# Optimization experiments

Hardware: AMD Instinct MI355X
Metric: run time of the kernel (lower is better)

## Reference

```python
import math
import jax, jax.numpy as jnp
import numpy as np

B, H, S, D = 2, 16, 2048, 64

def setup_inputs() -> dict:
    key = jax.random.key(0)
    kq, kk, kv = jax.random.split(key, 3)
    return {
        "query": jax.random.normal(kq, (B, H, S, D), dtype=jnp.float32),
        "key": jax.random.normal(kk, (B, H, S, D), dtype=jnp.float32),
        "value": jax.random.normal(kv, (B, H, S, D), dtype=jnp.float32),
        "mask": jnp.ones((B, S, 1), dtype=jnp.float32),  # padding mask, 1 = keep
        "mask_now": 0,  # 0 -> causal (tril diag=0); 1 -> strict causal (diag=-1)
    }

def reference(query, key, value, mask, mask_now):
    d_k = query.shape[-1]
    seq_len = mask.shape[1]
    # [B,H,S,S] scaled scores
    attn_scores = jnp.einsum("bhqd,bhkd->bhqk", query, key) / math.sqrt(d_k)
    diag = -1 if mask_now else 0
    triu_mask = jnp.tril(jnp.ones((seq_len, seq_len), dtype=mask.dtype), diag)  # [S,S]
    # mask[:, :, 0] -> per-query padding mask broadcast over key dim: [B,1,S,S]
    full_mask = triu_mask[None, None, :, :] * mask[:, None, :, 0:1]
    attn_scores = jnp.where(full_mask == 0, jnp.float32(-1e9), attn_scores)
    attn_scores = jax.nn.softmax(attn_scores, axis=-1)
    output = jnp.einsum("bhqk,bhkd->bhqd", attn_scores, value)
    return (output, attn_scores)
```

## Files before the change

### kernel.cpp

```cpp
#include <hip/hip_runtime.h>
#include <math.h>

#define NB 2
#define NH 16
#define SL 2048
#define DD 64
#define KC 64
#define NCH (SL / KC)
#define NT 256
#define LPS 68

typedef short bf16x8 __attribute__((ext_vector_type(8)));
typedef float f32x4  __attribute__((ext_vector_type(4)));

__device__ __forceinline__ unsigned short f2bf(float x) {
    unsigned u = __float_as_uint(x);
    u += 0x7fffu + ((u >> 16) & 1u);
    return (unsigned short)(u >> 16);
}

__device__ __forceinline__ void lds_barrier() {
    asm volatile("s_waitcnt lgkmcnt(0)\n\ts_barrier" ::: "memory");
}

__global__ __launch_bounds__(256)
void cvt_bf16(const float* __restrict__ in, unsigned short* __restrict__ out,
              int n4, float scale)
{
    int i = blockIdx.x * 256 + threadIdx.x;
    if (i >= n4) return;
    float4 v = ((const float4*)in)[i];
    ushort4 o;
    o.x = f2bf(v.x * scale); o.y = f2bf(v.y * scale);
    o.z = f2bf(v.z * scale); o.w = f2bf(v.w * scale);
    ((ushort4*)out)[i] = o;
}

__global__ __launch_bounds__(256)
void transpose_v(const float* __restrict__ V, unsigned short* __restrict__ Vt)
{
    __shared__ __align__(16) unsigned short vt[64 * 72];
    const int bh = blockIdx.x >> 5;
    const int s0 = (blockIdx.x & 31) * 64;
    const int t  = threadIdx.x;

    const float4* src = (const float4*)(V + ((size_t)bh * SL + s0) * DD);
    #pragma unroll
    for (int i = 0; i < 4; ++i) {
        int idx = t + i * 256;
        int r = idx >> 4, d4 = idx & 15;
        float4 v = src[r * 16 + d4];
        vt[(d4 * 4 + 0) * 72 + r] = f2bf(v.x);
        vt[(d4 * 4 + 1) * 72 + r] = f2bf(v.y);
        vt[(d4 * 4 + 2) * 72 + r] = f2bf(v.z);
        vt[(d4 * 4 + 3) * 72 + r] = f2bf(v.w);
    }
    __syncthreads();
    const int d = t >> 2, seg = t & 3;
    unsigned short* dst = Vt + ((size_t)bh * DD + d) * SL + s0 + seg * 16;
    uint4 p0 = *(const uint4*)&vt[d * 72 + seg * 16];
    uint4 p1 = *(const uint4*)&vt[d * 72 + seg * 16 + 8];
    *(uint4*)dst = p0;
    *(uint4*)(dst + 8) = p1;
}

__global__ __launch_bounds__(NT, 8)
void attn_mfma(const unsigned short* __restrict__ Qb,
               const unsigned short* __restrict__ Kb,
               const unsigned short* __restrict__ Vt,
               const float* __restrict__ Mg,
               const int* __restrict__ MNg,
               float* __restrict__ Og)
{
    __shared__ __align__(16) float ps[4][16 * LPS];
    __shared__ float lsx[4][16];

    const int tid  = threadIdx.x;
    const int w    = tid >> 6;
    const int lane = tid & 63;
    const int l15  = lane & 15;
    const int qd   = lane >> 4;

    const int lin  = blockIdx.x;
    const int xcd  = lin & 7;
    const int iloc = lin >> 3;
    const int bh   = xcd * 4 + (iloc >> 6);
    const int g    = iloc & 63;
    const int j    = (iloc >> 5) & 7;
    const int b    = bh >> 4;

    const int role  = (w + j) & 3;
    const int khalf = role & 1;
    const int r0    = (role < 2) ? g * 16 : 2032 - g * 16;

    const int diag = (MNg[0] != 0) ? -1 : 0;

    int rlim[4]; int anyDeg = 0;
    #pragma unroll
    for (int reg = 0; reg < 4; ++reg) {
        int row = r0 + qd * 4 + reg;
        float m = Mg[(size_t)b * SL + row];
        int rl = row + diag;
        if (m == 0.0f) rl = -1;
        rlim[reg] = rl;
        anyDeg |= (rl < 0);
    }
    const bool grpDeg = __any(anyDeg);
    const int lastB = grpDeg ? (NCH - 1) : ((r0 + 15 + diag) >> 6);
    const int N     = lastB + 1;
    const int kcMid = N >> 1;
    const int kcBeg = khalf ? kcMid : 0;
    const int kcEnd = khalf ? N : kcMid;

    const unsigned short* Qh  = Qb + (size_t)bh * SL * DD;
    const unsigned short* Kh  = Kb + (size_t)bh * SL * DD;
    const unsigned short* Vth = Vt + (size_t)bh * DD * SL;
    float* Oo   = Og + ((size_t)bh * SL + r0) * DD;
    float* Sout = Og + (size_t)NB * NH * SL * DD
                     + (size_t)bh * SL * SL + (size_t)r0 * SL;
    float* slab = ps[role];

    const unsigned short* qrow = Qh + (size_t)(r0 + l15) * DD + qd * 8;
    bf16x8 qf0 = *(const bf16x8*)qrow;
    bf16x8 qf1 = *(const bf16x8*)(qrow + 32);

    float lacc[4] = {0.0f, 0.0f, 0.0f, 0.0f};
    for (int it = kcBeg * 4; it < kcEnd * 4; ++it) {
        const unsigned short* kr = Kh + (size_t)(it * 16 + l15) * DD + qd * 8;
        bf16x8 f0 = *(const bf16x8*)kr;
        bf16x8 f1 = *(const bf16x8*)(kr + 32);
        f32x4 acc = {0.0f, 0.0f, 0.0f, 0.0f};
        __builtin_amdgcn_s_setprio(1);
        acc = __builtin_amdgcn_mfma_f32_16x16x32_bf16(qf0, f0, acc, 0, 0, 0);
        acc = __builtin_amdgcn_mfma_f32_16x16x32_bf16(qf1, f1, acc, 0, 0, 0);
        __builtin_amdgcn_s_setprio(0);
        const int col = it * 16 + l15;
        #pragma unroll
        for (int reg = 0; reg < 4; ++reg)
            lacc[reg] += (col <= rlim[reg]) ? __builtin_exp2f(acc[reg]) : 0.0f;
    }

    float lsum[4];
    #pragma unroll
    for (int reg = 0; reg < 4; ++reg) {
        float s = lacc[reg];
        s += __shfl_xor(s, 1);  s += __shfl_xor(s, 2);
        s += __shfl_xor(s, 4);  s += __shfl_xor(s, 8);
        lsum[reg] = s;
    }
    if (l15 == 0) {
        #pragma unroll
        for (int reg = 0; reg < 4; ++reg)
            lsx[role][qd * 4 + reg] = lsum[reg];
    }
    lds_barrier();
    float pmul[4], pfill[4];
    #pragma unroll
    for (int reg = 0; reg < 4; ++reg) {
        float tot = lsum[reg] + lsx[role ^ 1][qd * 4 + reg];
        pmul[reg]  = (rlim[reg] < 0) ? 0.0f : 1.0f / tot;
        pfill[reg] = (rlim[reg] < 0) ? (1.0f / (float)SL) : 0.0f;
    }

    f32x4 oacc[4];
    #pragma unroll
    for (int nt = 0; nt < 4; ++nt) oacc[nt] = (f32x4){0.0f, 0.0f, 0.0f, 0.0f};

    for (int kc = kcBeg; kc < kcEnd; ++kc) {
        const int c0 = kc * KC;
        #pragma unroll
        for (int nt = 0; nt < 4; ++nt) {
            const unsigned short* kr = Kh + (size_t)(c0 + nt * 16 + l15) * DD + qd * 8;
            bf16x8 f0 = *(const bf16x8*)kr;
            bf16x8 f1 = *(const bf16x8*)(kr + 32);
            f32x4 acc = {0.0f, 0.0f, 0.0f, 0.0f};
            __builtin_amdgcn_s_setprio(1);
            acc = __builtin_amdgcn_mfma_f32_16x16x32_bf16(qf0, f0, acc, 0, 0, 0);
            acc = __builtin_amdgcn_mfma_f32_16x16x32_bf16(qf1, f1, acc, 0, 0, 0);
            __builtin_amdgcn_s_setprio(0);
            const int col = c0 + nt * 16 + l15;
            #pragma unroll
            for (int reg = 0; reg < 4; ++reg) {
                float val = (col <= rlim[reg]) ? __builtin_exp2f(acc[reg]) * pmul[reg]
                                               : pfill[reg];
                slab[(qd * 4 + reg) * LPS + nt * 16 + l15] = val;
            }
        }
        #pragma unroll
        for (int ii = 0; ii < 4; ++ii) {
            int idx = ii * 64 + lane;
            int rr = idx >> 4, c4 = idx & 15;
            *(float4*)(Sout + (size_t)rr * SL + c0 + c4 * 4) =
                *(const float4*)&slab[rr * LPS + c4 * 4];
        }
        bf16x8 paf[2];
        #pragma unroll
        for (int kb = 0; kb < 2; ++kb) {
            const float* pr = &slab[l15 * LPS + kb * 32 + qd * 8];
            float4 x = *(const float4*)pr;
            float4 y = *(const float4*)(pr + 4);
            bf16x8 f;
            f[0] = (short)f2bf(x.x); f[1] = (short)f2bf(x.y);
            f[2] = (short)f2bf(x.z); f[3] = (short)f2bf(x.w);
            f[4] = (short)f2bf(y.x); f[5] = (short)f2bf(y.y);
            f[6] = (short)f2bf(y.z); f[7] = (short)f2bf(y.w);
            paf[kb] = f;
        }
        #pragma unroll
        for (int nt = 0; nt < 4; ++nt) {
            const unsigned short* vr = Vth + (size_t)(nt * 16 + l15) * SL + c0 + qd * 8;
            bf16x8 v0 = *(const bf16x8*)vr;
            bf16x8 v1 = *(const bf16x8*)(vr + 32);
            __builtin_amdgcn_s_setprio(1);
            oacc[nt] = __builtin_amdgcn_mfma_f32_16x16x32_bf16(paf[0], v0, oacc[nt], 0, 0, 0);
            oacc[nt] = __builtin_amdgcn_mfma_f32_16x16x32_bf16(paf[1], v1, oacc[nt], 0, 0, 0);
            __builtin_amdgcn_s_setprio(0);
        }
    }

    {
        const int zc0 = N * KC;
        const int rbeg = khalf * 8;
        float4 z = make_float4(0.0f, 0.0f, 0.0f, 0.0f);
        for (int rr = rbeg; rr < rbeg + 8; ++rr) {
            float* rowp = Sout + (size_t)rr * SL;
            for (int c = zc0 + (lane << 2); c < SL; c += 256)
                *(float4*)(rowp + c) = z;
        }
    }

    #pragma unroll
    for (int nt = 0; nt < 4; ++nt)
        #pragma unroll
        for (int reg = 0; reg < 4; ++reg)
            slab[(qd * 4 + reg) * LPS + nt * 16 + l15] = oacc[nt][reg];
    lds_barrier();
    {
        const float* sA = ps[role & ~1];
        const float* sB = ps[role | 1];
        #pragma unroll
        for (int ii = 0; ii < 2; ++ii) {
            int idx = ii * 64 + lane;
            int rr = (idx >> 4) + khalf * 8;
            int c4 = idx & 15;
            float4 a = *(const float4*)&sA[rr * LPS + c4 * 4];
            float4 bv = *(const float4*)&sB[rr * LPS + c4 * 4];
            float4 o = make_float4(a.x + bv.x, a.y + bv.y, a.z + bv.z, a.w + bv.w);
            *(float4*)(Oo + (size_t)rr * DD + c4 * 4) = o;
        }
    }
}

extern "C" void kernel_launch(void* const* d_in, const int* in_sizes, int n_in,
                              void* d_out, int out_size, void* d_ws, size_t ws_size,
                              hipStream_t stream)
{
    const float* q  = (const float*)d_in[0];
    const float* k  = (const float*)d_in[1];
    const float* v  = (const float*)d_in[2];
    const float* mk = (const float*)d_in[3];
    const int*   mn = (const int*)d_in[4];
    float* out = (float*)d_out;

    const size_t nElem = (size_t)NB * NH * SL * DD;
    unsigned short* Qb = (unsigned short*)d_ws;
    unsigned short* Kp = Qb + nElem;
    unsigned short* Vp = Kp + nElem;

    const int n4 = (int)(nElem / 4);
    cvt_bf16<<<n4 / 256, 256, 0, stream>>>(q, Qb, n4, 0.125f * 1.44269504f);
    cvt_bf16<<<n4 / 256, 256, 0, stream>>>(k, Kp, n4, 1.0f);
    transpose_v<<<NB * NH * (SL / 64), 256, 0, stream>>>(v, Vp);

    attn_mfma<<<2048, NT, 0, stream>>>(Qb, Kp, Vp, mk, mn, out);
}
```

Measured before the change: 802.0 us.

## Restructure attention into 32-row blocks with 256-column chunks and split PV output

Each block now processes two 32-row query tiles (a front and a mirrored back tile for causal balance) instead of four independent 16-row wave roles. The four waves split into row halves and column halves: QK^T uses 256-wide key chunks shared through a larger LDS slab, and PV splits the output head dimension across waves. This removes the per-wave partial-output reduction and enlarges key/value reuse, and K loads are double-buffered. The cost is more LDS per block, lower occupancy (launch bound 4), extra barriers, and coarser causal granularity, so more masked work is done near the diagonal.

Result: faster. 735.6 us (-8.3%).

```diff
diff --git a/kernel.cpp b/kernel.cpp
--- a/kernel.cpp
+++ b/kernel.cpp
@@ -5,10 +5,8 @@
 #define NH 16
 #define SL 2048
 #define DD 64
-#define KC 64
-#define NCH (SL / KC)
 #define NT 256
-#define LPS 68
+#define SLABW 268
 
 typedef short bf16x8 __attribute__((ext_vector_type(8)));
 typedef float f32x4  __attribute__((ext_vector_type(4)));
@@ -64,7 +62,7 @@
     *(uint4*)(dst + 8) = p1;
 }
 
-__global__ __launch_bounds__(NT, 8)
+__global__ __launch_bounds__(NT, 4)
 void attn_mfma(const unsigned short* __restrict__ Qb,
                const unsigned short* __restrict__ Kb,
                const unsigned short* __restrict__ Vt,
@@ -72,7 +70,7 @@
                const int* __restrict__ MNg,
                float* __restrict__ Og)
 {
-    __shared__ __align__(16) float ps[4][16 * LPS];
+    __shared__ __align__(16) float slab[32 * SLABW];
     __shared__ float lsx[4][16];
 
     const int tid  = threadIdx.x;
@@ -80,174 +78,192 @@
     const int lane = tid & 63;
     const int l15  = lane & 15;
     const int qd   = lane >> 4;
+    const int rowhalf = w >> 1;
+    const int colhalf = w & 1;
 
     const int lin  = blockIdx.x;
     const int xcd  = lin & 7;
     const int iloc = lin >> 3;
-    const int bh   = xcd * 4 + (iloc >> 6);
-    const int g    = iloc & 63;
-    const int j    = (iloc >> 5) & 7;
+    const int g    = iloc & 31;
+    const int bh   = xcd * 4 + (iloc >> 5);
     const int b    = bh >> 4;
 
-    const int role  = (w + j) & 3;
-    const int khalf = role & 1;
-    const int r0    = (role < 2) ? g * 16 : 2032 - g * 16;
-
     const int diag = (MNg[0] != 0) ? -1 : 0;
-
-    int rlim[4]; int anyDeg = 0;
-    #pragma unroll
-    for (int reg = 0; reg < 4; ++reg) {
-        int row = r0 + qd * 4 + reg;
-        float m = Mg[(size_t)b * SL + row];
-        int rl = row + diag;
-        if (m == 0.0f) rl = -1;
-        rlim[reg] = rl;
-        anyDeg |= (rl < 0);
-    }
-    const bool grpDeg = __any(anyDeg);
-    const int lastB = grpDeg ? (NCH - 1) : ((r0 + 15 + diag) >> 6);
-    const int N     = lastB + 1;
-    const int kcMid = N >> 1;
-    const int kcBeg = khalf ? kcMid : 0;
-    const int kcEnd = khalf ? N : kcMid;
 
     const unsigned short* Qh  = Qb + (size_t)bh * SL * DD;
     const unsigned short* Kh  = Kb + (size_t)bh * SL * DD;
     const unsigned short* Vth = Vt + (size_t)bh * DD * SL;
-    float* Oo   = Og + ((size_t)bh * SL + r0) * DD;
-    float* Sout = Og + (size_t)NB * NH * SL * DD
-                     + (size_t)bh * SL * SL + (size_t)r0 * SL;
-    float* slab = ps[role];
-
-    const unsigned short* qrow = Qh + (size_t)(r0 + l15) * DD + qd * 8;
-    bf16x8 qf0 = *(const bf16x8*)qrow;
-    bf16x8 qf1 = *(const bf16x8*)(qrow + 32);
-
-    float lacc[4] = {0.0f, 0.0f, 0.0f, 0.0f};
-    for (int it = kcBeg * 4; it < kcEnd * 4; ++it) {
-        const unsigned short* kr = Kh + (size_t)(it * 16 + l15) * DD + qd * 8;
-        bf16x8 f0 = *(const bf16x8*)kr;
-        bf16x8 f1 = *(const bf16x8*)(kr + 32);
-        f32x4 acc = {0.0f, 0.0f, 0.0f, 0.0f};
-        __builtin_amdgcn_s_setprio(1);
-        acc = __builtin_amdgcn_mfma_f32_16x16x32_bf16(qf0, f0, acc, 0, 0, 0);
-        acc = __builtin_amdgcn_mfma_f32_16x16x32_bf16(qf1, f1, acc, 0, 0, 0);
-        __builtin_amdgcn_s_setprio(0);
-        const int col = it * 16 + l15;
-        #pragma unroll
-        for (int reg = 0; reg < 4; ++reg)
-            lacc[reg] += (col <= rlim[reg]) ? __builtin_exp2f(acc[reg]) : 0.0f;
-    }
-
-    float lsum[4];
-    #pragma unroll
-    for (int reg = 0; reg < 4; ++reg) {
-        float s = lacc[reg];
-        s += __shfl_xor(s, 1);  s += __shfl_xor(s, 2);
-        s += __shfl_xor(s, 4);  s += __shfl_xor(s, 8);
-        lsum[reg] = s;
-    }
-    if (l15 == 0) {
-        #pragma unroll
-        for (int reg = 0; reg < 4; ++reg)
-            lsx[role][qd * 4 + reg] = lsum[reg];
-    }
-    lds_barrier();
-    float pmul[4], pfill[4];
-    #pragma unroll
-    for (int reg = 0; reg < 4; ++reg) {
-        float tot = lsum[reg] + lsx[role ^ 1][qd * 4 + reg];
-        pmul[reg]  = (rlim[reg] < 0) ? 0.0f : 1.0f / tot;
-        pfill[reg] = (rlim[reg] < 0) ? (1.0f / (float)SL) : 0.0f;
-    }
-
-    f32x4 oacc[4];
-    #pragma unroll
-    for (int nt = 0; nt < 4; ++nt) oacc[nt] = (f32x4){0.0f, 0.0f, 0.0f, 0.0f};
-
-    for (int kc = kcBeg; kc < kcEnd; ++kc) {
-        const int c0 = kc * KC;
-        #pragma unroll
-        for (int nt = 0; nt < 4; ++nt) {
-            const unsigned short* kr = Kh + (size_t)(c0 + nt * 16 + l15) * DD + qd * 8;
-            bf16x8 f0 = *(const bf16x8*)kr;
-            bf16x8 f1 = *(const bf16x8*)(kr + 32);
-            f32x4 acc = {0.0f, 0.0f, 0.0f, 0.0f};
-            __builtin_amdgcn_s_setprio(1);
-            acc = __builtin_amdgcn_mfma_f32_16x16x32_bf16(qf0, f0, acc, 0, 0, 0);
-            acc = __builtin_amdgcn_mfma_f32_16x16x32_bf16(qf1, f1, acc, 0, 0, 0);
-            __builtin_amdgcn_s_setprio(0);
-            const int col = c0 + nt * 16 + l15;
-            #pragma unroll
-            for (int reg = 0; reg < 4; ++reg) {
-                float val = (col <= rlim[reg]) ? __builtin_exp2f(acc[reg]) * pmul[reg]
-                                               : pfill[reg];
-                slab[(qd * 4 + reg) * LPS + nt * 16 + l15] = val;
-            }
-        }
-        #pragma unroll
-        for (int ii = 0; ii < 4; ++ii) {
-            int idx = ii * 64 + lane;
-            int rr = idx >> 4, c4 = idx & 15;
-            *(float4*)(Sout + (size_t)rr * SL + c0 + c4 * 4) =
-                *(const float4*)&slab[rr * LPS + c4 * 4];
-        }
-        bf16x8 paf[2];
-        #pragma unroll
-        for (int kb = 0; kb < 2; ++kb) {
-            const float* pr = &slab[l15 * LPS + kb * 32 + qd * 8];
-            float4 x = *(const float4*)pr;
-            float4 y = *(const float4*)(pr + 4);
-            bf16x8 f;
-            f[0] = (short)f2bf(x.x); f[1] = (short)f2bf(x.y);
-            f[2] = (short)f2bf(x.z); f[3] = (short)f2bf(x.w);
-            f[4] = (short)f2bf(y.x); f[5] = (short)f2bf(y.y);
-            f[6] = (short)f2bf(y.z); f[7] = (short)f2bf(y.w);
-            paf[kb] = f;
-        }
-        #pragma unroll
-        for (int nt = 0; nt < 4; ++nt) {
-            const unsigned short* vr = Vth + (size_t)(nt * 16 + l15) * SL + c0 + qd * 8;
-            bf16x8 v0 = *(const bf16x8*)vr;
-            bf16x8 v1 = *(const bf16x8*)(vr + 32);
-            __builtin_amdgcn_s_setprio(1);
-            oacc[nt] = __builtin_amdgcn_mfma_f32_16x16x32_bf16(paf[0], v0, oacc[nt], 0, 0, 0);
-            oacc[nt] = __builtin_amdgcn_mfma_f32_16x16x32_bf16(paf[1], v1, oacc[nt], 0, 0, 0);
-            __builtin_amdgcn_s_setprio(0);
-        }
-    }
-
-    {
-        const int zc0 = N * KC;
-        const int rbeg = khalf * 8;
-        float4 z = make_float4(0.0f, 0.0f, 0.0f, 0.0f);
-        for (int rr = rbeg; rr < rbeg + 8; ++rr) {
-            float* rowp = Sout + (size_t)rr * SL;
-            for (int c = zc0 + (lane << 2); c < SL; c += 256)
-                *(float4*)(rowp + c) = z;
-        }
-    }
-
-    #pragma unroll
-    for (int nt = 0; nt < 4; ++nt)
-        #pragma unroll
-        for (int reg = 0; reg < 4; ++reg)
-            slab[(qd * 4 + reg) * LPS + nt * 16 + l15] = oacc[nt][reg];
-    lds_barrier();
-    {
-        const float* sA = ps[role & ~1];
-        const float* sB = ps[role | 1];
+    float* Sb = Og + (size_t)NB * NH * SL * DD + (size_t)bh * SL * SL;
+    float* Ob = Og + (size_t)bh * SL * DD;
+
+    for (int sweep = 0; sweep < 2; ++sweep) {
+        const int R0 = sweep ? (2016 - g * 32) : (g * 32);
+
+        int degflag = 0;
+        if (lane < 32) {
+            int row = R0 + lane;
+            float m = Mg[(size_t)b * SL + row];
+            degflag = (m == 0.0f) || (row + diag < 0);
+        }
+        const bool deg32 = __any(degflag);
+        const int M = deg32 ? 8 : (((R0 + 31 + diag) >> 8) + 1);
+
+        int rlim[4];
+        #pragma unroll
+        for (int reg = 0; reg < 4; ++reg) {
+            int row = R0 + rowhalf * 16 + qd * 4 + reg;
+            float m = Mg[(size_t)b * SL + row];
+            int rl = row + diag;
+            if (m == 0.0f) rl = -1;
+            rlim[reg] = rl;
+        }
+
+        const unsigned short* qrow = Qh + (size_t)(R0 + rowhalf * 16 + l15) * DD + qd * 8;
+        bf16x8 qf0 = *(const bf16x8*)qrow;
+        bf16x8 qf1 = *(const bf16x8*)(qrow + 32);
+
+        auto ldK = [&](int ct, bf16x8& f0, bf16x8& f1) {
+            const unsigned short* kr = Kh + (size_t)(ct + l15) * DD + qd * 8;
+            f0 = *(const bf16x8*)kr;
+            f1 = *(const bf16x8*)(kr + 32);
+        };
+
+        float lacc[4] = {0.0f, 0.0f, 0.0f, 0.0f};
+        {
+            auto cmpA = [&](int ct, bf16x8 f0, bf16x8 f1) {
+                f32x4 acc = {0.0f, 0.0f, 0.0f, 0.0f};
+                __builtin_amdgcn_s_setprio(1);
+                acc = __builtin_amdgcn_mfma_f32_16x16x32_bf16(qf0, f0, acc, 0, 0, 0);
+                acc = __builtin_amdgcn_mfma_f32_16x16x32_bf16(qf1, f1, acc, 0, 0, 0);
+                __builtin_amdgcn_s_setprio(0);
+                const int col = ct + l15;
+                #pragma unroll
+                for (int reg = 0; reg < 4; ++reg)
+                    lacc[reg] += (col <= rlim[reg]) ? __builtin_exp2f(acc[reg]) : 0.0f;
+            };
+            auto tcol = [&](int t) {
+                return ((t >> 3) << 8) + colhalf * 128 + ((t & 7) << 4);
+            };
+            const int T = M * 8;
+            bf16x8 A0, A1, B0, B1;
+            ldK(tcol(0), A0, A1);
+            for (int t = 0; t < T; t += 2) {
+                ldK(tcol(t + 1), B0, B1);
+                cmpA(tcol(t), A0, A1);
+                if (t + 2 < T) ldK(tcol(t + 2), A0, A1);
+                cmpA(tcol(t + 1), B0, B1);
+            }
+        }
+
+        float lsum[4];
+        #pragma unroll
+        for (int reg = 0; reg < 4; ++reg) {
+            float s = lacc[reg];
+            s += __shfl_xor(s, 1);  s += __shfl_xor(s, 2);
+            s += __shfl_xor(s, 4);  s += __shfl_xor(s, 8);
+            lsum[reg] = s;
+        }
+        if (l15 == 0) {
+            #pragma unroll
+            for (int reg = 0; reg < 4; ++reg)
+                lsx[w][qd * 4 + reg] = lsum[reg];
+        }
+        lds_barrier();
+        float pmul[4], pfill[4];
+        #pragma unroll
+        for (int reg = 0; reg < 4; ++reg) {
+            float tot = lsum[reg] + lsx[w ^ 1][qd * 4 + reg];
+            pmul[reg]  = (rlim[reg] < 0) ? 0.0f : 1.0f / tot;
+            pfill[reg] = (rlim[reg] < 0) ? (1.0f / (float)SL) : 0.0f;
+        }
+
+        f32x4 oacc[2];
+        oacc[0] = (f32x4){0.0f, 0.0f, 0.0f, 0.0f};
+        oacc[1] = (f32x4){0.0f, 0.0f, 0.0f, 0.0f};
+
+        for (int mc = 0; mc < M; ++mc) {
+            const int C0 = mc << 8;
+            {
+                bf16x8 a0, a1, b0, b1;
+                ldK(C0 + colhalf * 128, a0, a1);
+                #pragma unroll
+                for (int t = 0; t < 8; ++t) {
+                    bf16x8 f0 = (t & 1) ? b0 : a0;
+                    bf16x8 f1 = (t & 1) ? b1 : a1;
+                    if (t < 7) {
+                        if (t & 1) ldK(C0 + colhalf * 128 + ((t + 1) << 4), a0, a1);
+                        else       ldK(C0 + colhalf * 128 + ((t + 1) << 4), b0, b1);
+                    }
+                    f32x4 acc = {0.0f, 0.0f, 0.0f, 0.0f};
+                    __builtin_amdgcn_s_setprio(1);
+                    acc = __builtin_amdgcn_mfma_f32_16x16x32_bf16(qf0, f0, acc, 0, 0, 0);
+                    acc = __builtin_amdgcn_mfma_f32_16x16x32_bf16(qf1, f1, acc, 0, 0, 0);
+                    __builtin_amdgcn_s_setprio(0);
+                    const int scol = colhalf * 128 + (t << 4) + l15;
+                    const int col  = C0 + scol;
+                    #pragma unroll
+                    for (int reg = 0; reg < 4; ++reg) {
+                        float val = (col <= rlim[reg]) ? __builtin_exp2f(acc[reg]) * pmul[reg]
+                                                       : pfill[reg];
+                        slab[(rowhalf * 16 + qd * 4 + reg) * SLABW + scol] = val;
+                    }
+                }
+            }
+            lds_barrier();
+            #pragma unroll
+            for (int i = 0; i < 8; ++i) {
+                int rr = w * 8 + i;
+                *(float4*)(Sb + (size_t)(R0 + rr) * SL + C0 + lane * 4) =
+                    *(const float4*)&slab[rr * SLABW + lane * 4];
+            }
+            #pragma unroll
+            for (int ks = 0; ks < 8; ++ks) {
+                const float* pr = &slab[(rowhalf * 16 + l15) * SLABW + ks * 32 + qd * 8];
+                float4 x = *(const float4*)pr;
+                float4 y = *(const float4*)(pr + 4);
+                bf16x8 f;
+                f[0] = (short)f2bf(x.x); f[1] = (short)f2bf(x.y);
+                f[2] = (short)f2bf(x.z); f[3] = (short)f2bf(x.w);
+                f[4] = (short)f2bf(y.x); f[5] = (short)f2bf(y.y);
+                f[6] = (short)f2bf(y.z); f[7] = (short)f2bf(y.w);
+                #pragma unroll
+                for (int nt = 0; nt < 2; ++nt) {
+                    const unsigned short* vr = Vth
+                        + (size_t)(colhalf * 32 + nt * 16 + l15) * SL + C0 + ks * 32 + qd * 8;
+                    bf16x8 v = *(const bf16x8*)vr;
+                    __builtin_amdgcn_s_setprio(1);
+                    oacc[nt] = __builtin_amdgcn_mfma_f32_16x16x32_bf16(f, v, oacc[nt], 0, 0, 0);
+                    __builtin_amdgcn_s_setprio(0);
+                }
+            }
+            lds_barrier();
+        }
+
+        {
+            const int zc0 = M << 8;
+            float4 z = make_float4(0.0f, 0.0f, 0.0f, 0.0f);
+            for (int i = 0; i < 8; ++i) {
+                float* rowp = Sb + (size_t)(R0 + w * 8 + i) * SL;
+                for (int c = zc0 + (lane << 2); c < SL; c += 256)
+                    *(float4*)(rowp + c) = z;
+            }
+        }
+
+        #pragma unroll
+        for (int nt = 0; nt < 2; ++nt)
+            #pragma unroll
+            for (int reg = 0; reg < 4; ++reg)
+                slab[(rowhalf * 16 + qd * 4 + reg) * SLABW + colhalf * 32 + nt * 16 + l15] =
+                    oacc[nt][reg];
+        lds_barrier();
         #pragma unroll
         for (int ii = 0; ii < 2; ++ii) {
-            int idx = ii * 64 + lane;
-            int rr = (idx >> 4) + khalf * 8;
-            int c4 = idx & 15;
-            float4 a = *(const float4*)&sA[rr * LPS + c4 * 4];
-            float4 bv = *(const float4*)&sB[rr * LPS + c4 * 4];
-            float4 o = make_float4(a.x + bv.x, a.y + bv.y, a.z + bv.z, a.w + bv.w);
-            *(float4*)(Oo + (size_t)rr * DD + c4 * 4) = o;
-        }
+            int rr = w * 8 + ii * 4 + (lane >> 4);
+            int c4 = lane & 15;
+            *(float4*)(Ob + (size_t)(R0 + rr) * DD + c4 * 4) =
+                *(const float4*)&slab[rr * SLABW + c4 * 4];
+        }
+        lds_barrier();
     }
 }
 
@@ -272,5 +288,5 @@
     cvt_bf16<<<n4 / 256, 256, 0, stream>>>(k, Kp, n4, 1.0f);
     transpose_v<<<NB * NH * (SL / 64), 256, 0, stream>>>(v, Vp);
 
-    attn_mfma<<<2048, NT, 0, stream>>>(Qb, Kp, Vp, mk, mn, out);
-}
+    attn_mfma<<<1024, NT, 0, stream>>>(Qb, Kp, Vp, mk, mn, out);
+}
```
